# Kernel tuning notes

Hardware: AMD Instinct MI355X
Metric: run time of the kernel (lower is better)

## Reference

```python
import jax, jax.numpy as jnp
import numpy as np

B, L, D, H, E, K = 4, 2048, 1024, 4096, 8, 2


def setup_inputs() -> dict:
    key = jax.random.key(0)
    ks = jax.random.split(key, 6)
    x = jax.random.normal(ks[0], (B, L, D), dtype=jnp.float32)
    expert_indices = jax.random.randint(ks[1], (B, L, K), 0, E, dtype=jnp.int64)
    expert_weights = jax.random.uniform(ks[2], (B, L, K), dtype=jnp.float32)
    # expert FFN params (2-layer SiLU MLP), scaled for stable magnitudes
    w1 = jax.random.normal(ks[3], (E, D, H), dtype=jnp.float32) * (1.0 / np.sqrt(D))
    b1 = jnp.zeros((E, H), dtype=jnp.float32)
    w2 = jax.random.normal(ks[4], (E, H, D), dtype=jnp.float32) * (1.0 / np.sqrt(H))
    b2 = jnp.zeros((E, D), dtype=jnp.float32)
    return {"x": x, "expert_indices": expert_indices, "expert_weights": expert_weights,
            "w1": w1, "b1": b1, "w2": w2, "b2": b2}


def reference(x, expert_indices, expert_weights, w1, b1, w2, b2):
    # Faithful to MoEDispatcher.forward with capacity_factor=inf (no dropping):
    # every expert's full FFN is run on ALL tokens, then mask-combined.
    num_experts = w1.shape[0]
    out = jnp.zeros_like(x)
    for e in range(num_experts):  # static loop over experts (matches original)
        mask = (expert_indices == e)                                    # [B,L,K]
        token_w = jnp.sum(expert_weights * mask.astype(x.dtype), -1)    # [B,L]
        h = jax.nn.silu(jnp.einsum('bld,dh->blh', x, w1[e]) + b1[e])    # [B,L,H]
        y = jnp.einsum('blh,hd->bld', h, w2[e]) + b2[e]                 # [B,L,D]
        out = out + y * token_w[..., None]
    return out
```

## Files before the change

### kernel.cpp

```cpp
#include <hip/hip_runtime.h>
#include <hip/hip_bf16.h>
#include <stdint.h>

#define TOKENS 8192
#define DDIM 1024
#define HDIM 4096
#define NEXP 8
#define MAXENT 16384
#define MAXTILES 72

typedef __attribute__((ext_vector_type(4))) float f32x4;
typedef __attribute__((ext_vector_type(8))) short bf16x8;
typedef __attribute__((ext_vector_type(4))) int i32x4;

__device__ __forceinline__ unsigned short f2bf(float f) {
  __hip_bfloat16 h = __float2bfloat16(f);
  return __builtin_bit_cast(unsigned short, h);
}

__device__ __forceinline__ void gload16(const void* g, void* l) {
  __builtin_amdgcn_global_load_lds(
      (const __attribute__((address_space(1))) unsigned int*)g,
      (__attribute__((address_space(3))) unsigned int*)l, 16, 0, 0);
}

__device__ __forceinline__ void bar0() {
  asm volatile("" ::: "memory");
  __builtin_amdgcn_s_barrier();
  asm volatile("" ::: "memory");
}

#define LGKM0 asm volatile("s_waitcnt lgkmcnt(0)" ::: "memory")
#define VMWAIT(N) asm volatile("s_waitcnt vmcnt(" #N ")" ::: "memory")


__global__ void moe_count(const int* __restrict__ idx, int* __restrict__ meta) {
  int t = blockIdx.x * 256 + threadIdx.x;
  if (t >= TOKENS) return;
  int e0 = idx[2 * t], e1 = idx[2 * t + 1];
  atomicAdd(&meta[e0], 1);
  if (e1 != e0) atomicAdd(&meta[e1], 1);
}

__global__ void moe_scan(int* __restrict__ meta) {
  if (threadIdx.x != 0 || blockIdx.x != 0) return;
  int s = 0;
  for (int e = 0; e < NEXP; ++e) { meta[16 + e] = s; meta[32 + e] = s; s += meta[e]; }
  meta[16 + NEXP] = s;
  int nt = 0;
  for (int e = 0; e < NEXP; ++e) {
    int m = (meta[e] + 255) >> 8;
    for (int t = 0; t < m; ++t) meta[64 + nt++] = e | (t << 8);
  }
  meta[48] = nt;
}

__global__ void moe_scatter(const int* __restrict__ idx, const float* __restrict__ ew,
                            int* __restrict__ meta, int* __restrict__ etok,
                            float* __restrict__ ewgt, int* __restrict__ inv) {
  int t = blockIdx.x * 256 + threadIdx.x;
  if (t >= TOKENS) return;
  int e0 = idx[2 * t], e1 = idx[2 * t + 1];
  float a = ew[2 * t], b = ew[2 * t + 1];
  if (e0 == e1) {
    int p = atomicAdd(&meta[32 + e0], 1);
    etok[p] = t; ewgt[p] = a + b;
    inv[2 * t] = p; inv[2 * t + 1] = -1;
  } else {
    int p = atomicAdd(&meta[32 + e0], 1);
    etok[p] = t; ewgt[p] = a;
    int q = atomicAdd(&meta[32 + e1], 1);
    etok[q] = t; ewgt[q] = b;
    inv[2 * t] = p; inv[2 * t + 1] = q;
  }
}


__global__ __launch_bounds__(256) void gather_pre(const float* __restrict__ x,
                                                  const int* __restrict__ etok,
                                                  const int* __restrict__ meta,
                                                  unsigned short* __restrict__ xgp) {
  int ntiles = meta[48];
  int page = blockIdx.x, kt = blockIdx.y;
  if (page >= ntiles) return;
  int te = meta[64 + page];
  int e = te & 255, mt = te >> 8;
  int ent0 = meta[16 + e] + mt * 256, lim = meta[16 + e + 1];
  int tid = threadIdx.x;
#pragma unroll
  for (int it = 0; it < 4; ++it) {
    int u = it * 256 + tid;
    int chunk = u >> 6, lane = u & 63;
    int ent = ent0 + chunk * 16 + (lane & 15);
    if (ent > lim - 1) ent = lim - 1;
    int tok = etok[ent];
    const float4* s = (const float4*)(x + (size_t)tok * DDIM + kt * 32 + ((lane >> 4) << 3));
    float4 a = s[0], b = s[1];
    union { unsigned short h[8]; i32x4 v; } o;
    o.h[0] = f2bf(a.x); o.h[1] = f2bf(a.y); o.h[2] = f2bf(a.z); o.h[3] = f2bf(a.w);
    o.h[4] = f2bf(b.x); o.h[5] = f2bf(b.y); o.h[6] = f2bf(b.z); o.h[7] = f2bf(b.w);
    ((i32x4*)xgp)[(size_t)(page * 32 + kt) * 1024 + u] = o.v;
  }
}

__global__ __launch_bounds__(256) void pretile_w(const float* __restrict__ src,
                                                 unsigned short* __restrict__ dst,
                                                 int Kdim, int Ndim) {
  __shared__ unsigned short t16[64][266];
  int NB = Ndim >> 8, KB = Kdim >> 6;
  int bid = blockIdx.x;
  int kblk = bid % KB; int rest = bid / KB;
  int nblk = rest % NB; int e = rest / NB;
  const float* s = src + ((size_t)e * Kdim + ((size_t)kblk << 6)) * Ndim + ((size_t)nblk << 8);
  int tid = threadIdx.x;
  int cp = tid & 127, rh = tid >> 7;
#pragma unroll
  for (int rr = 0; rr < 32; ++rr) {
    int r = rh * 32 + rr;
    float2 v = *(const float2*)(s + (size_t)r * Ndim + 2 * cp);
    unsigned int pk = (unsigned int)f2bf(v.x) | ((unsigned int)f2bf(v.y) << 16);
    *(unsigned int*)&t16[r][2 * cp] = pk;
  }
  __syncthreads();
  int KT32 = Kdim >> 5;
#pragma unroll
  for (int it = 0; it < 8; ++it) {
    int u = it * 256 + tid;
    int kt2 = u >> 10, rem = u & 1023;
    int chunk = rem >> 6, lane = rem & 63;
    int nl = chunk * 16 + (lane & 15);
    int kl = kt2 * 32 + ((lane >> 4) << 3);
    union { unsigned short h[8]; i32x4 v; } o;
#pragma unroll
    for (int i = 0; i < 8; ++i) o.h[i] = t16[kl + i][nl];
    size_t idx = (((size_t)e * NB + nblk) * KT32 + kblk * 2 + kt2) * 1024 + rem;
    ((i32x4*)dst)[idx] = o.v;
  }
}


template <int MODE>
__global__ __launch_bounds__(512, 2) void moe_gemm(
    const unsigned short* __restrict__ Apre,
    const unsigned short* __restrict__ Bpre,
    const float* __restrict__ bias,
    const int* __restrict__ meta,
    const float* __restrict__ ewgt,
    unsigned short* __restrict__ Hbuf,
    float* __restrict__ Ybuf,
    int AKT, int BtNT, int BtKT, int ntg0, int kt0B,
    int nk, int biasOff, int bstr, int sIsZero, int KT_H) {
  const int* offsets = meta + 16;
  int ntiles = meta[48];
  int NX = gridDim.x;
  int lid = blockIdx.x + NX * blockIdx.y;
  int Ntot = NX * ntiles;
  if (lid >= Ntot) return;
  int q = Ntot >> 3, r = Ntot & 7;
  int xcd = lid & 7, pos = lid >> 3;
  int nlid = (xcd < r ? xcd * (q + 1) : r * (q + 1) + (xcd - r) * q) + pos;
  int nt = nlid / ntiles;
  int mti = nlid - nt * ntiles;
  int te = meta[64 + mti];
  int e = te & 255, mt = te >> 8;
  int off = offsets[e], cnt = offsets[e + 1] - off;

  __shared__ __align__(128) char lds[131072];

  int tid = threadIdx.x, lane = tid & 63, wid = tid >> 6;
  int wr = wid >> 2, wc = wid & 3;
  int fr = lane & 15, fu = lane >> 4;

  const char* srcA = (const char*)Apre + ((size_t)mti * AKT << 14) + (tid << 4);
  const char* srcB = (const char*)Bpre +
      ((((size_t)e * BtNT + ntg0 + nt) * BtKT + kt0B) << 14) + (tid << 4);

#define STAGE_A(Tn) do { \
    char* _d = lds + (((Tn) & 3) << 14) + (tid << 4); \
    const char* _s = srcA + ((size_t)(Tn) << 14); \
    gload16(_s, _d); gload16(_s + 8192, _d + 8192); } while (0)
#define STAGE_B(Tn) do { \
    char* _d = lds + 65536 + (((Tn) & 3) << 14) + (tid << 4); \
    const char* _s = srcB + ((size_t)(Tn) << 14); \
    gload16(_s, _d); gload16(_s + 8192, _d + 8192); } while (0)

  f32x4 acc[8][4];
#pragma unroll
  for (int m = 0; m < 8; ++m)
#pragma unroll
    for (int n = 0; n < 4; ++n) acc[m][n] = (f32x4){0.f, 0.f, 0.f, 0.f};

  STAGE_A(0); STAGE_B(0);
  STAGE_A(1); STAGE_B(1);
  STAGE_A(2); STAGE_B(2);
  VMWAIT(8);
  bar0();

  for (int kt = 0; kt < nk; ++kt) {
    const char* pa = lds + ((kt & 3) << 14) + (wr << 13) + (lane << 4);
    const char* pb = lds + 65536 + ((kt & 3) << 14) + (wc << 12) + (lane << 4);
    bool st = (kt + 3 < nk);

    bf16x8 a0 = *(const bf16x8*)(pa);
    bf16x8 a1 = *(const bf16x8*)(pa + 1024);
    bf16x8 a2 = *(const bf16x8*)(pa + 2048);
    bf16x8 a3 = *(const bf16x8*)(pa + 3072);
    bf16x8 bg[4];
#pragma unroll
    for (int n = 0; n < 4; ++n) bg[n] = *(const bf16x8*)(pb + n * 1024);
    if (st) STAGE_A(kt + 3);
    bar0();
    LGKM0;
    __builtin_amdgcn_s_setprio(1);
#pragma unroll
    for (int n = 0; n < 4; ++n) {
      acc[0][n] = __builtin_amdgcn_mfma_f32_16x16x32_bf16(a0, bg[n], acc[0][n], 0, 0, 0);
      acc[1][n] = __builtin_amdgcn_mfma_f32_16x16x32_bf16(a1, bg[n], acc[1][n], 0, 0, 0);
      acc[2][n] = __builtin_amdgcn_mfma_f32_16x16x32_bf16(a2, bg[n], acc[2][n], 0, 0, 0);
      acc[3][n] = __builtin_amdgcn_mfma_f32_16x16x32_bf16(a3, bg[n], acc[3][n], 0, 0, 0);
    }
    __builtin_amdgcn_s_setprio(0);
    bar0();

    a0 = *(const bf16x8*)(pa + 4096);
    a1 = *(const bf16x8*)(pa + 5120);
    a2 = *(const bf16x8*)(pa + 6144);
    a3 = *(const bf16x8*)(pa + 7168);
    if (st) STAGE_B(kt + 3);
    bar0();
    LGKM0;
    __builtin_amdgcn_s_setprio(1);
#pragma unroll
    for (int n = 0; n < 4; ++n) {
      acc[4][n] = __builtin_amdgcn_mfma_f32_16x16x32_bf16(a0, bg[n], acc[4][n], 0, 0, 0);
      acc[5][n] = __builtin_amdgcn_mfma_f32_16x16x32_bf16(a1, bg[n], acc[5][n], 0, 0, 0);
      acc[6][n] = __builtin_amdgcn_mfma_f32_16x16x32_bf16(a2, bg[n], acc[6][n], 0, 0, 0);
      acc[7][n] = __builtin_amdgcn_mfma_f32_16x16x32_bf16(a3, bg[n], acc[7][n], 0, 0, 0);
    }
    __builtin_amdgcn_s_setprio(0);
    if (kt < nk - 3)       { VMWAIT(8); }
    else if (kt == nk - 3) { VMWAIT(4); }
    else if (kt == nk - 2) { VMWAIT(0); }
    bar0();
  }
#undef STAGE_A
#undef STAGE_B

  if (MODE == 0) {
    unsigned short* page = Hbuf + (size_t)mti * KT_H * 8192;
#pragma unroll
    for (int m = 0; m < 8; ++m) {
#pragma unroll
      for (int r = 0; r < 4; ++r) {
        int row = wr * 128 + m * 16 + fu * 4 + r;
        int gm = mt * 256 + row;
        if (gm < cnt) {
#pragma unroll
          for (int n = 0; n < 4; ++n) {
            int lc = nt * 256 + wc * 64 + n * 16 + fr;
            float v = acc[m][n][r] + bias[e * bstr + biasOff + lc];
            v = v / (1.f + __expf(-v));
            int kt = lc >> 5;
            int idx = (((kt * 16 + (row >> 4)) << 9) +
                       (((row & 15) + (((lc >> 3) & 3) << 4)) << 3) + (lc & 7));
            page[idx] = f2bf(v);
          }
        }
      }
    }
  } else {
#pragma unroll
    for (int m = 0; m < 8; ++m) {
#pragma unroll
      for (int r = 0; r < 4; ++r) {
        int row = wr * 128 + m * 16 + fu * 4 + r;
        int gm = mt * 256 + row;
        if (gm < cnt) {
          int ent = off + gm;
          float wgt = ewgt[ent];
          float* yrow = Ybuf + (size_t)ent * DDIM;
#pragma unroll
          for (int n = 0; n < 4; ++n) {
            int col = nt * 256 + wc * 64 + n * 16 + fr;
            float v = acc[m][n][r];
            if (sIsZero) {
              yrow[col] = (v + bias[e * bstr + col]) * wgt;
            } else {
              yrow[col] += v * wgt;
            }
          }
        }
      }
    }
  }
}


__global__ __launch_bounds__(256) void combine(const float* __restrict__ yb,
                                               const int* __restrict__ inv,
                                               float* __restrict__ out) {
  int t = blockIdx.x, c = threadIdx.x;
  int p = inv[2 * t], q2 = inv[2 * t + 1];
  float4 v = ((const float4*)(yb + (size_t)p * DDIM))[c];
  if (q2 >= 0) {
    float4 w = ((const float4*)(yb + (size_t)q2 * DDIM))[c];
    v.x += w.x; v.y += w.y; v.z += w.z; v.w += w.w;
  }
  ((float4*)(out + (size_t)t * DDIM))[c] = v;
}


extern "C" void kernel_launch(void* const* d_in, const int* in_sizes, int n_in,
                              void* d_out, int out_size, void* d_ws, size_t ws_size,
                              hipStream_t stream) {
  (void)in_sizes; (void)n_in; (void)out_size;
  const float* x = (const float*)d_in[0];
  const int* eidx = (const int*)d_in[1];
  const float* ew = (const float*)d_in[2];
  const float* w1 = (const float*)d_in[3];
  const float* b1 = (const float*)d_in[4];
  const float* w2 = (const float*)d_in[5];
  const float* b2 = (const float*)d_in[6];
  float* out = (float*)d_out;

  char* w = (char*)d_ws;
  size_t o_meta = 0;
  size_t o_etok = 4096;
  size_t o_ewgt = o_etok + (size_t)MAXENT * 4;
  size_t o_inv  = o_ewgt + (size_t)MAXENT * 4;
  size_t o_xgp  = o_inv + (size_t)TOKENS * 2 * 4;
  size_t o_w1t  = o_xgp + (size_t)MAXTILES * 32 * 16384;
  size_t o_w2t  = o_w1t + (size_t)NEXP * DDIM * HDIM * 2;
  size_t o_yb   = o_w2t + (size_t)NEXP * DDIM * HDIM * 2;
  size_t o_h    = o_yb + (size_t)MAXENT * DDIM * 4;

  int S = 1;
  while (S < 16) {
    size_t need = o_h + (size_t)MAXTILES * ((HDIM / S) >> 5) * 16384;
    if (need <= ws_size) break;
    S *= 2;
  }
  int HC = HDIM / S;
  int KT_H = HC >> 5;

  int* meta = (int*)(w + o_meta);
  int* etok = (int*)(w + o_etok);
  float* ewgt = (float*)(w + o_ewgt);
  int* inv = (int*)(w + o_inv);
  unsigned short* xgp = (unsigned short*)(w + o_xgp);
  unsigned short* w1t = (unsigned short*)(w + o_w1t);
  unsigned short* w2t = (unsigned short*)(w + o_w2t);
  float* ybuf = (float*)(w + o_yb);
  unsigned short* hbuf = (unsigned short*)(w + o_h);

  hipMemsetAsync(w + o_meta, 0, 4096, stream);

  moe_count<<<TOKENS / 256, 256, 0, stream>>>(eidx, meta);
  moe_scan<<<1, 64, 0, stream>>>(meta);
  moe_scatter<<<TOKENS / 256, 256, 0, stream>>>(eidx, ew, meta, etok, ewgt, inv);
  gather_pre<<<dim3(MAXTILES, DDIM / 32), 256, 0, stream>>>(x, etok, meta, xgp);
  pretile_w<<<NEXP * (HDIM >> 8) * (DDIM >> 6), 256, 0, stream>>>(w1, w1t, DDIM, HDIM);
  pretile_w<<<NEXP * (DDIM >> 8) * (HDIM >> 6), 256, 0, stream>>>(w2, w2t, HDIM, DDIM);

  for (int s = 0; s < S; ++s) {
    moe_gemm<0><<<dim3(HC / 256, MAXTILES), 512, 0, stream>>>(
        xgp, w1t, b1, meta, ewgt, hbuf, nullptr,
         DDIM >> 5,  HDIM >> 8,  DDIM >> 5,
         (s * HC) >> 8,  0,
         DDIM >> 5,  s * HC,  HDIM, 1, KT_H);
    moe_gemm<1><<<dim3(DDIM / 256, MAXTILES), 512, 0, stream>>>(
        hbuf, w2t, b2, meta, ewgt, nullptr, ybuf,
         KT_H,  DDIM >> 8,  HDIM >> 5,
         0,  (s * HC) >> 5,
         KT_H,  0,  DDIM, (s == 0) ? 1 : 0, KT_H);
  }
  combine<<<TOKENS, 256, 0, stream>>>(ybuf, inv, out);
}
```

Before: 563.8 us.

## Load B operand directly into registers, halve LDS, restructure A pipeline

```diff
diff --git a/kernel.cpp b/kernel.cpp
--- a/kernel.cpp
+++ b/kernel.cpp
@@ -30,7 +30,6 @@
   asm volatile("" ::: "memory");
 }
 
-#define LGKM0 asm volatile("s_waitcnt lgkmcnt(0)" ::: "memory")
 #define VMWAIT(N) asm volatile("s_waitcnt vmcnt(" #N ")" ::: "memory")
 
 
@@ -138,6 +137,24 @@
   }
 }
 
+
+#define LOADB(R0, R1, R2, R3, KT) do {                 \
+    const char* _p = pB + ((size_t)(KT) << 14);        \
+    R0 = *(const bf16x8*)(_p);                         \
+    R1 = *(const bf16x8*)(_p + 1024);                  \
+    R2 = *(const bf16x8*)(_p + 2048);                  \
+    R3 = *(const bf16x8*)(_p + 3072); } while (0)
+
+#define MFMA32(PA, B0_, B1_, B2_, B3_) do {            \
+    __builtin_amdgcn_s_setprio(1);                     \
+    _Pragma("unroll") for (int m = 0; m < 8; ++m) {    \
+      bf16x8 a_ = *(const bf16x8*)((PA) + m * 1024);   \
+      acc[m][0] = __builtin_amdgcn_mfma_f32_16x16x32_bf16(a_, B0_, acc[m][0], 0, 0, 0); \
+      acc[m][1] = __builtin_amdgcn_mfma_f32_16x16x32_bf16(a_, B1_, acc[m][1], 0, 0, 0); \
+      acc[m][2] = __builtin_amdgcn_mfma_f32_16x16x32_bf16(a_, B2_, acc[m][2], 0, 0, 0); \
+      acc[m][3] = __builtin_amdgcn_mfma_f32_16x16x32_bf16(a_, B3_, acc[m][3], 0, 0, 0); \
+    }                                                  \
+    __builtin_amdgcn_s_setprio(0); } while (0)
 
 template <int MODE>
 __global__ __launch_bounds__(512, 2) void moe_gemm(
@@ -165,24 +182,20 @@
   int e = te & 255, mt = te >> 8;
   int off = offsets[e], cnt = offsets[e + 1] - off;
 
-  __shared__ __align__(128) char lds[131072];
+  __shared__ __align__(128) char lds[65536];
 
   int tid = threadIdx.x, lane = tid & 63, wid = tid >> 6;
   int wr = wid >> 2, wc = wid & 3;
   int fr = lane & 15, fu = lane >> 4;
 
   const char* srcA = (const char*)Apre + ((size_t)mti * AKT << 14) + (tid << 4);
-  const char* srcB = (const char*)Bpre +
-      ((((size_t)e * BtNT + ntg0 + nt) * BtKT + kt0B) << 14) + (tid << 4);
+  const char* pB = (const char*)Bpre +
+      ((((size_t)e * BtNT + ntg0 + nt) * BtKT + kt0B) << 14) + ((wc * 4) << 10) + (lane << 4);
 
 #define STAGE_A(Tn) do { \
     char* _d = lds + (((Tn) & 3) << 14) + (tid << 4); \
     const char* _s = srcA + ((size_t)(Tn) << 14); \
     gload16(_s, _d); gload16(_s + 8192, _d + 8192); } while (0)
-#define STAGE_B(Tn) do { \
-    char* _d = lds + 65536 + (((Tn) & 3) << 14) + (tid << 4); \
-    const char* _s = srcB + ((size_t)(Tn) << 14); \
-    gload16(_s, _d); gload16(_s + 8192, _d + 8192); } while (0)
 
   f32x4 acc[8][4];
 #pragma unroll
@@ -190,61 +203,33 @@
 #pragma unroll
     for (int n = 0; n < 4; ++n) acc[m][n] = (f32x4){0.f, 0.f, 0.f, 0.f};
 
-  STAGE_A(0); STAGE_B(0);
-  STAGE_A(1); STAGE_B(1);
-  STAGE_A(2); STAGE_B(2);
-  VMWAIT(8);
+  bf16x8 bx0, bx1, bx2, bx3, by0, by1, by2, by3;
+
+  STAGE_A(0); STAGE_A(1);
+  LOADB(bx0, bx1, bx2, bx3, 0);
+  VMWAIT(0);
   bar0();
 
-  for (int kt = 0; kt < nk; ++kt) {
-    const char* pa = lds + ((kt & 3) << 14) + (wr << 13) + (lane << 4);
-    const char* pb = lds + 65536 + ((kt & 3) << 14) + (wc << 12) + (lane << 4);
-    bool st = (kt + 3 < nk);
-
-    bf16x8 a0 = *(const bf16x8*)(pa);
-    bf16x8 a1 = *(const bf16x8*)(pa + 1024);
-    bf16x8 a2 = *(const bf16x8*)(pa + 2048);
-    bf16x8 a3 = *(const bf16x8*)(pa + 3072);
-    bf16x8 bg[4];
-#pragma unroll
-    for (int n = 0; n < 4; ++n) bg[n] = *(const bf16x8*)(pb + n * 1024);
-    if (st) STAGE_A(kt + 3);
+  for (int kt = 0; kt < nk; kt += 2) {
+    LOADB(by0, by1, by2, by3, kt + 1);
+    if (kt + 2 < nk) STAGE_A(kt + 2);
+    {
+      const char* pa = lds + ((kt & 3) << 14) + (wr << 13) + (lane << 4);
+      MFMA32(pa, bx0, bx1, bx2, bx3);
+    }
+    VMWAIT(2);
     bar0();
-    LGKM0;
-    __builtin_amdgcn_s_setprio(1);
-#pragma unroll
-    for (int n = 0; n < 4; ++n) {
-      acc[0][n] = __builtin_amdgcn_mfma_f32_16x16x32_bf16(a0, bg[n], acc[0][n], 0, 0, 0);
-      acc[1][n] = __builtin_amdgcn_mfma_f32_16x16x32_bf16(a1, bg[n], acc[1][n], 0, 0, 0);
-      acc[2][n] = __builtin_amdgcn_mfma_f32_16x16x32_bf16(a2, bg[n], acc[2][n], 0, 0, 0);
-      acc[3][n] = __builtin_amdgcn_mfma_f32_16x16x32_bf16(a3, bg[n], acc[3][n], 0, 0, 0);
+
+    if (kt + 2 < nk) LOADB(bx0, bx1, bx2, bx3, kt + 2);
+    if (kt + 3 < nk) STAGE_A(kt + 3);
+    {
+      const char* pa = lds + (((kt + 1) & 3) << 14) + (wr << 13) + (lane << 4);
+      MFMA32(pa, by0, by1, by2, by3);
     }
-    __builtin_amdgcn_s_setprio(0);
+    VMWAIT(2);
     bar0();
-
-    a0 = *(const bf16x8*)(pa + 4096);
-    a1 = *(const bf16x8*)(pa + 5120);
-    a2 = *(const bf16x8*)(pa + 6144);
-    a3 = *(const bf16x8*)(pa + 7168);
-    if (st) STAGE_B(kt + 3);
-    bar0();
-    LGKM0;
-    __builtin_amdgcn_s_setprio(1);
-#pragma unroll
-    for (int n = 0; n < 4; ++n) {
-      acc[4][n] = __builtin_amdgcn_mfma_f32_16x16x32_bf16(a0, bg[n], acc[4][n], 0, 0, 0);
-      acc[5][n] = __builtin_amdgcn_mfma_f32_16x16x32_bf16(a1, bg[n], acc[5][n], 0, 0, 0);
-      acc[6][n] = __builtin_amdgcn_mfma_f32_16x16x32_bf16(a2, bg[n], acc[6][n], 0, 0, 0);
-      acc[7][n] = __builtin_amdgcn_mfma_f32_16x16x32_bf16(a3, bg[n], acc[7][n], 0, 0, 0);
-    }
-    __builtin_amdgcn_s_setprio(0);
-    if (kt < nk - 3)       { VMWAIT(8); }
-    else if (kt == nk - 3) { VMWAIT(4); }
-    else if (kt == nk - 2) { VMWAIT(0); }
-    bar0();
   }
 #undef STAGE_A
-#undef STAGE_B
 
   if (MODE == 0) {
     unsigned short* page = Hbuf + (size_t)mti * KT_H * 8192;
```

Measured after the change: 639.7 us. 13.5% more time.
